# Performance work log

Measured on AMD Instinct MI355X. Metric: run time of the kernel, lower is better.

Reference implementation:

```python
import jax, jax.numpy as jnp
import numpy as np

N = 8192
E = 262144
IN_DIM = 128
OUT_DIM = 16


def _linear_params(key, fan_in, fan_out):
    k1, k2 = jax.random.split(key)
    bound = 1.0 / np.sqrt(fan_in)
    W = jax.random.uniform(k1, (fan_in, fan_out), jnp.float32, -bound, bound)
    b = jax.random.uniform(k2, (fan_out,), jnp.float32, -bound, bound)
    return W, b


def setup_inputs() -> dict:
    key = jax.random.key(0)
    ks = jax.random.split(key, 10)
    x = jax.random.normal(ks[0], (N, IN_DIM), jnp.float32)
    edge_index = jax.random.randint(ks[1], (2, E), 0, N, jnp.int64)
    W1, b1 = _linear_params(ks[2], IN_DIM, 128)
    W2, b2 = _linear_params(ks[3], 128, 256)
    W3, b3 = _linear_params(ks[4], 256, 64)
    Wk, bk = _linear_params(ks[5], 256, 256)
    Wq, bq = _linear_params(ks[6], 256, 256)
    Wr, br = _linear_params(ks[7], IN_DIM, 64)
    Wf, bf = _linear_params(ks[8], 64, OUT_DIM)
    ln_g = jnp.ones((64,), jnp.float32)
    ln_b = jnp.zeros((64,), jnp.float32)
    return dict(x=x, edge_index=edge_index, W1=W1, b1=b1, W2=W2, b2=b2,
                W3=W3, b3=b3, Wk=Wk, bk=bk, Wq=Wq, bq=bq, Wr=Wr, br=br,
                ln_g=ln_g, ln_b=ln_b, Wf=Wf, bf=bf)


def gcn_conv(x, W, b, row, col, n):
    # PyG GCNConv: add self-loops, symmetric normalization, aggregate src->dst
    xw = x @ W                                          # [N, F_out]
    loops = jnp.arange(n, dtype=row.dtype)
    r = jnp.concatenate([row, loops])
    c = jnp.concatenate([col, loops])
    deg = jax.ops.segment_sum(jnp.ones_like(c, jnp.float32), c, num_segments=n)
    dinv = jnp.where(deg > 0, jax.lax.rsqrt(jnp.maximum(deg, 1e-12)), 0.0)
    norm = dinv[r] * dinv[c]                            # [E+N]
    out = jax.ops.segment_sum(norm[:, None] * xw[r], c, num_segments=n)
    return out + b


def _forward(x, edge_index, W1, b1, W2, b2, W3, b3, Wk, bk, Wq, bq,
             Wr, br, ln_g, ln_b, Wf, bf):
    row, col = edge_index[0], edge_index[1]
    n = x.shape[0]
    residual = x @ Wr + br                              # [N, 64]
    h = jax.nn.leaky_relu(gcn_conv(x, W1, b1, row, col, n))   # dropout = eval no-op
    h = jax.nn.leaky_relu(gcn_conv(h, W2, b2, row, col, n))   # [N, 256]
    keys = h @ Wk + bk
    queries = h @ Wq + bq
    scores = queries @ keys.T                           # [N, N] dense, as in source
    mask = jnp.zeros((n, n), jnp.float32).at[row, col].set(1.0)
    scores = scores * mask                              # multiplicative mask (faithful)
    attn = jax.nn.softmax(scores, axis=-1)
    h = attn @ h                                        # [N, 256]
    h = jax.nn.leaky_relu(gcn_conv(h, W3, b3, row, col, n))   # [N, 64]
    z = h + residual
    mu = jnp.mean(z, axis=-1, keepdims=True)
    var = jnp.mean((z - mu) ** 2, axis=-1, keepdims=True)
    z = (z - mu) * jax.lax.rsqrt(var + 1e-5) * ln_g + ln_b
    pooled = jnp.max(z, axis=0)                         # 'max' pooling -> [64]
    return pooled @ Wf + bf                             # [OUT_DIM]


def reference(x, edge_index, W1, b1, W2, b2, W3, b3, Wk, bk, Wq, bq,
              Wr, br, ln_g, ln_b, Wf, bf):
    return _forward(x, edge_index, W1, b1, W2, b2, W3, b3, Wk, bk, Wq, bq,
                    Wr, br, ln_g, ln_b, Wf, bf)
```

## Files before the change

### kernel.cpp

```cpp
#include <hip/hip_runtime.h>
#include <hip/hip_fp16.h>
#include <cstdint>
#include <cstddef>

#define NNODES 8192
#define NEDGES 262144
#define MAXDEG 96
#define SMEM_BYTES 10496

typedef _Float16 f16x8 __attribute__((ext_vector_type(8)));
typedef _Float16 h2v   __attribute__((ext_vector_type(2)));
typedef float    f32x4 __attribute__((ext_vector_type(4)));

__device__ __forceinline__ float leaky(float v){ return v > 0.f ? v : 0.01f*v; }

__device__ __forceinline__ unsigned fmap(float f){
  unsigned u = __float_as_uint(f);
  return (u & 0x80000000u) ? ~u : (u | 0x80000000u);
}
__device__ __forceinline__ float funmap(unsigned u){
  return (u & 0x80000000u) ? __uint_as_float(u & 0x7FFFFFFFu) : __uint_as_float(~u);
}
__device__ __forceinline__ h2v as_h2(unsigned u){
  union{ unsigned x; h2v h; } c; c.x = u; return c.h;
}

struct GP {
  const float *x; const int *ei;
  const float *W1,*b1,*W2,*b2,*W3,*b3,*Wk,*bk,*Wq,*bq,*Wr,*br,*lng,*lnb,*Wf,*bfv;
  float* out;
  __half *xw1h,*h1h,*h1ah,*h2h,*qth,*gh,*hw3h;
  float *resid,*sw3;
  __half *Wqkt,*W2t,*W3t;
  float *bqk,*wb,*s0p;
  int *degc,*degr,*csrc,*csrd;
  unsigned* poolpart;
};

__device__ __forceinline__ void gemm_tile(const __half* __restrict__ A,
    const __half* __restrict__ Bt, const float* __restrict__ bias,
    float* __restrict__ Cf, __half* __restrict__ Ch, float* __restrict__ csum,
    int K, int N, int act, int bx, int by,
    _Float16 (*As)[40], _Float16 (*Bs)[40], float* cs){
  int t = threadIdx.x, w = t>>6, lane = t&63;
  int m0 = bx*64, n0 = by*64;
  int quad = lane>>4, l15 = lane&15;
  int srow = t>>2, soff = (t&3)*8;
  f32x4 acc0 = {0.f,0.f,0.f,0.f}, acc1 = acc0, acc2 = acc0, acc3 = acc0;
  for (int k0 = 0; k0 < K; k0 += 32){
    *(uint4*)&As[srow][soff] = *(const uint4*)(A  + (size_t)(m0+srow)*K + k0 + soff);
    *(uint4*)&Bs[srow][soff] = *(const uint4*)(Bt + (size_t)(n0+srow)*K + k0 + soff);
    __syncthreads();
    f16x8 af = *(const f16x8*)&As[w*16 + l15][quad*8];
    f16x8 b0 = *(const f16x8*)&Bs[ 0 + l15][quad*8];
    f16x8 b1 = *(const f16x8*)&Bs[16 + l15][quad*8];
    f16x8 b2 = *(const f16x8*)&Bs[32 + l15][quad*8];
    f16x8 b3 = *(const f16x8*)&Bs[48 + l15][quad*8];
    acc0 = __builtin_amdgcn_mfma_f32_16x16x32_f16(af, b0, acc0, 0,0,0);
    acc1 = __builtin_amdgcn_mfma_f32_16x16x32_f16(af, b1, acc1, 0,0,0);
    acc2 = __builtin_amdgcn_mfma_f32_16x16x32_f16(af, b2, acc2, 0,0,0);
    acc3 = __builtin_amdgcn_mfma_f32_16x16x32_f16(af, b3, acc3, 0,0,0);
    __syncthreads();
  }
  f32x4 accs[4] = {acc0, acc1, acc2, acc3};
  if (csum){
    if (t < 64) cs[t] = 0.f;
    __syncthreads();
    #pragma unroll
    for (int nt=0; nt<4; ++nt){
      float pp = accs[nt][0]+accs[nt][1]+accs[nt][2]+accs[nt][3];
      atomicAdd(&cs[nt*16 + l15], pp);
    }
    __syncthreads();
    if (t < 64) atomicAdd(&csum[n0 + t], cs[t]);
  }
  #pragma unroll
  for (int nt=0; nt<4; ++nt){
    int col = n0 + nt*16 + l15;
    float bv = bias ? bias[col] : 0.f;
    #pragma unroll
    for (int r=0;r<4;r++){
      int row = m0 + w*16 + quad*4 + r;
      float v = accs[nt][r] + bv;
      if (act) v = leaky(v);
      if (Cf) Cf[(size_t)row*N + col] = v;
      if (Ch) Ch[(size_t)row*N + col] = __float2half(v);
    }
  }
}

template<int TRANSB>
__device__ __forceinline__ void gemm_f32(const float* __restrict__ A,
    const float* __restrict__ B, const float* __restrict__ bias,
    float* __restrict__ Cf, __half* __restrict__ Ch,
    int K, int N, int bx, int by,
    _Float16 (*As)[40], _Float16 (*Bs)[40]){
  int t = threadIdx.x, w = t>>6, lane = t&63;
  int m0 = bx*64, n0 = by*64;
  int quad = lane>>4, l15 = lane&15;
  int srow = t>>2, soff = (t&3)*8;
  f32x4 acc0 = {0.f,0.f,0.f,0.f}, acc1 = acc0, acc2 = acc0, acc3 = acc0;
  for (int k0 = 0; k0 < K; k0 += 32){
    float4 a0 = *(const float4*)(A + (size_t)(m0+srow)*K + k0 + soff);
    float4 a1 = *(const float4*)(A + (size_t)(m0+srow)*K + k0 + soff + 4);
    _Float16* ad = &As[srow][soff];
    ad[0]=(_Float16)a0.x; ad[1]=(_Float16)a0.y; ad[2]=(_Float16)a0.z; ad[3]=(_Float16)a0.w;
    ad[4]=(_Float16)a1.x; ad[5]=(_Float16)a1.y; ad[6]=(_Float16)a1.z; ad[7]=(_Float16)a1.w;
    _Float16* bd = &Bs[srow][soff];
    if (TRANSB){
      #pragma unroll
      for (int u=0;u<8;u++)
        bd[u] = (_Float16)B[(size_t)(k0+soff+u)*N + n0+srow];
    } else {
      float4 b0 = *(const float4*)(B + (size_t)(n0+srow)*K + k0 + soff);
      float4 b1 = *(const float4*)(B + (size_t)(n0+srow)*K + k0 + soff + 4);
      bd[0]=(_Float16)b0.x; bd[1]=(_Float16)b0.y; bd[2]=(_Float16)b0.z; bd[3]=(_Float16)b0.w;
      bd[4]=(_Float16)b1.x; bd[5]=(_Float16)b1.y; bd[6]=(_Float16)b1.z; bd[7]=(_Float16)b1.w;
    }
    __syncthreads();
    f16x8 af = *(const f16x8*)&As[w*16 + l15][quad*8];
    f16x8 b0 = *(const f16x8*)&Bs[ 0 + l15][quad*8];
    f16x8 b1 = *(const f16x8*)&Bs[16 + l15][quad*8];
    f16x8 b2 = *(const f16x8*)&Bs[32 + l15][quad*8];
    f16x8 b3 = *(const f16x8*)&Bs[48 + l15][quad*8];
    acc0 = __builtin_amdgcn_mfma_f32_16x16x32_f16(af, b0, acc0, 0,0,0);
    acc1 = __builtin_amdgcn_mfma_f32_16x16x32_f16(af, b1, acc1, 0,0,0);
    acc2 = __builtin_amdgcn_mfma_f32_16x16x32_f16(af, b2, acc2, 0,0,0);
    acc3 = __builtin_amdgcn_mfma_f32_16x16x32_f16(af, b3, acc3, 0,0,0);
    __syncthreads();
  }
  f32x4 accs[4] = {acc0, acc1, acc2, acc3};
  #pragma unroll
  for (int nt=0; nt<4; ++nt){
    int col = n0 + nt*16 + l15;
    float bv = bias ? bias[col] : 0.f;
    #pragma unroll
    for (int r=0;r<4;r++){
      int row = m0 + w*16 + quad*4 + r;
      float v = accs[nt][r] + bv;
      if (Cf) Cf[(size_t)row*N + col] = v;
      if (Ch) Ch[(size_t)row*N + col] = __float2half(v);
    }
  }
}

template<int INS, int OUTS, int ACT>
__device__ __forceinline__ void agg128w(const __half* __restrict__ in,
    const int* __restrict__ deg, const int* __restrict__ src,
    __half* __restrict__ outp, const float* __restrict__ bias, int i){
  int lane = threadIdx.x & 63;
  int dcc = deg[i];
  float dc = rsqrtf((float)(dcc+1));
  int e0 = i*MAXDEG, e1 = e0 + dcc;
  float2 acc = make_float2(0.f, 0.f);
  for (int eb = e0; eb < e1; eb += 8){
    int m = e1 - eb; if (m > 8) m = 8;
    int r[8];
    #pragma unroll
    for (int u=0;u<8;u++) r[u] = src[(u<m) ? eb+u : eb];
    __half2 hv[8]; float sc[8];
    #pragma unroll
    for (int u=0;u<8;u++){
      hv[u] = *(const __half2*)(in + (size_t)r[u]*128 + lane*2);
      sc[u] = INS ? 1.f : rsqrtf((float)(deg[r[u]]+1));
    }
    #pragma unroll
    for (int u=0;u<8;u++){
      if (u < m){
        float2 h = __half22float2(hv[u]);
        if (INS){ acc.x += h.x; acc.y += h.y; }
        else { acc.x = fmaf(sc[u], h.x, acc.x); acc.y = fmaf(sc[u], h.y, acc.y); }
      }
    }
  }
  float2 self = __half22float2(*(const __half2*)(in + (size_t)i*128 + lane*2));
  float ss = INS ? 1.f : dc;
  float ox = dc*(ss*self.x + acc.x);
  float oy = dc*(ss*self.y + acc.y);
  if (ACT){
    ox = leaky(ox + bias[lane*2]);
    oy = leaky(oy + bias[lane*2+1]);
  }
  if (OUTS){ ox *= dc; oy *= dc; }
  *(__half2*)(outp + (size_t)i*128 + lane*2) = __floats2half2_rn(ox, oy);
}

__device__ __forceinline__ void attn_unit(const GP& p, int u){
  const int n = NNODES;
  int w = threadIdx.x>>6, lane = threadIdx.x&63;
  int i = u*4 + w;
  int fo = lane*4;
  uint2 qtu = *(const uint2*)(p.qth + (size_t)i*256 + fo);
  h2v q0 = as_h2(qtu.x), q1 = as_h2(qtu.y);
  float4 wbv = *(const float4*)(p.wb + fo);
  uint2 hiu  = *(const uint2*)(p.h2h + (size_t)i*256 + fo);
  float2 hia = __half22float2(*(__half2*)&hiu.x);
  float2 hib = __half22float2(*(__half2*)&hiu.y);
  float pv = hia.x*wbv.x + hia.y*wbv.y + hib.x*wbv.z + hib.y*wbv.w;
  #pragma unroll
  for (int mm=32; mm; mm>>=1) pv += __shfl_xor(pv, mm, 64);
  float base = pv + p.s0p[0];
  int dri = p.degr[i];
  int e0 = i*MAXDEG, e1 = e0 + dri;
  float acc = 0.f, dsum = 0.f;
  int slot = lane & 7;
  for (int eb = e0; eb < e1; eb += 8){
    int m = e1 - eb; if (m > 8) m = 8;
    int j[8];
    #pragma unroll
    for (int u8=0;u8<8;u8++) j[u8] = p.csrd[(u8<m) ? eb+u8 : eb];
    uint2 hv[8]; float gv[8];
    #pragma unroll
    for (int u8=0;u8<8;u8++){
      hv[u8] = *(const uint2*)(p.h2h + (size_t)j[u8]*256 + fo);
      gv[u8] = __half2float(p.gh[(size_t)j[u8]*64 + lane]);
    }
    float d[8];
    #pragma unroll
    for (int u8=0;u8<8;u8++)
      d[u8] = __builtin_amdgcn_fdot2(q1, as_h2(hv[u8].y),
              __builtin_amdgcn_fdot2(q0, as_h2(hv[u8].x), 0.f, false), false);
    #pragma unroll
    for (int v=0;v<8;v++) d[v] += __shfl_xor(d[v], 1, 64);
    float e0_ = (lane&1) ? d[1] : d[0];
    float e1_ = (lane&1) ? d[3] : d[2];
    float e2_ = (lane&1) ? d[5] : d[4];
    float e3_ = (lane&1) ? d[7] : d[6];
    e0_ += __shfl_xor(e0_, 2, 64);  e1_ += __shfl_xor(e1_, 2, 64);
    e2_ += __shfl_xor(e2_, 2, 64);  e3_ += __shfl_xor(e3_, 2, 64);
    float f0_ = (lane&2) ? e1_ : e0_;
    float f1_ = (lane&2) ? e3_ : e2_;
    f0_ += __shfl_xor(f0_, 4, 64);  f1_ += __shfl_xor(f1_, 4, 64);
    float g_ = (lane&4) ? f1_ : f0_;
    g_ += __shfl_xor(g_,  8, 64);
    g_ += __shfl_xor(g_, 16, 64);
    g_ += __shfl_xor(g_, 32, 64);
    float wep = __expf(g_ + base);
    float wm = (slot < m) ? wep : 0.f;
    wm += __shfl_xor(wm, 1, 64);
    wm += __shfl_xor(wm, 2, 64);
    wm += __shfl_xor(wm, 4, 64);
    dsum += wm;
    #pragma unroll
    for (int u8=0;u8<8;u8++){
      if (u8 < m){
        float wu = __shfl(wep, u8, 64);
        acc = fmaf(wu - 1.f, gv[u8], acc);
      }
    }
  }
  float inv = 1.0f / ((float)(n - dri) + dsum);
  float di = rsqrtf((float)(p.degc[i]+1));
  p.hw3h[(size_t)i*64 + lane] = __float2half(di * (p.sw3[lane] + acc) * inv);
}

__device__ __forceinline__ unsigned zp_val(const GP& p, int c){
  int lane = threadIdx.x & 63;
  int dcc = p.degc[c];
  float dc = rsqrtf((float)(dcc+1));
  float acc = 0.f;
  int e0 = c*MAXDEG, e1 = e0 + dcc;
  for (int eb = e0; eb < e1; eb += 8){
    int m = e1 - eb; if (m > 8) m = 8;
    int r[8];
    #pragma unroll
    for (int u=0;u<8;u++) r[u] = p.csrc[(u<m) ? eb+u : eb];
    __half hval[8];
    #pragma unroll
    for (int u=0;u<8;u++) hval[u] = p.hw3h[(size_t)r[u]*64 + lane];
    #pragma unroll
    for (int u=0;u<8;u++)
      if (u < m) acc += __half2float(hval[u]);
  }
  float self = __half2float(p.hw3h[(size_t)c*64 + lane]);
  float v = leaky(dc*(self + acc) + p.b3[lane]) + p.resid[(size_t)c*64 + lane];
  float s = v;
  #pragma unroll
  for (int mm=32; mm; mm>>=1) s += __shfl_xor(s, mm, 64);
  float mu = s * (1.0f/64.0f);
  float d = v - mu;
  float s2 = d*d;
  #pragma unroll
  for (int mm=32; mm; mm>>=1) s2 += __shfl_xor(s2, mm, 64);
  float zv = d * rsqrtf(s2*(1.0f/64.0f) + 1e-5f) * p.lng[lane] + p.lnb[lane];
  return fmap(zv);
}

__device__ __forceinline__ void final_unit(const GP& p, char* smem){
  int t = threadIdx.x, f = t & 63, g = t >> 6;
  unsigned (*sm)[64] = (unsigned(*)[64])smem;
  float* pool = (float*)(smem + 1024);
  unsigned mu = 0u;
  for (int b = g; b < 64; b += 4) mu = max(mu, p.poolpart[b*64 + f]);
  sm[g][f] = mu;
  __syncthreads();
  if (g == 0)
    pool[f] = funmap(max(max(sm[0][f],sm[1][f]), max(sm[2][f],sm[3][f])));
  __syncthreads();
  if (t < 16){
    float a = p.bfv[t];
    #pragma unroll
    for (int ff=0; ff<64; ++ff) a = fmaf(pool[ff], p.Wf[ff*16 + t], a);
    p.out[t] = a;
  }
}

__global__ __launch_bounds__(256) void k_z(GP p){
  __shared__ float smv[768];
  int b = blockIdx.x, t = threadIdx.x;
  if (b < 16){
    int idx = b*256 + t;
    int4 z = {0,0,0,0};
    ((int4*)p.degc)[idx] = z;
  } else if (b < 144){
    int idx = (b-16)*256 + t;
    int nn = idx >> 7, k = idx & 127;
    p.W2t[idx] = __float2half(p.W2[k*256 + nn]);
  } else if (b < 208){
    int idx = (b-144)*256 + t;
    int nn = idx >> 8, k = idx & 255;
    p.W3t[idx] = __float2half(p.W3[k*64 + nn]);
  } else if (b < 224){
    p.poolpart[(b-208)*256 + t] = 0u;
  } else if (b == 224){
    if (t < 64) p.sw3[t] = 0.f;
  } else {
    int c = b - 225;
    float* ra = smv; float* rb = smv + 256; float* rc = smv + 512;
    ra[t] = p.Wk[c*256 + t] * p.bq[t];
    rb[t] = p.Wq[c*256 + t] * p.bk[t];
    if (c == 0) rc[t] = p.bq[t]*p.bk[t];
    __syncthreads();
    for (int off=128; off; off>>=1){
      if (t < off){
        ra[t] += ra[t+off];
        rb[t] += rb[t+off];
        if (c == 0) rc[t] += rc[t+off];
      }
      __syncthreads();
    }
    if (t == 0){
      p.bqk[c] = ra[0];
      p.wb[c]  = rb[0];
      if (c == 0) p.s0p[0] = rc[0];
    }
  }
}

__global__ __launch_bounds__(256) void k_pre(GP p){
  __shared__ __align__(16) char smem[SMEM_BYTES];
  _Float16 (*As)[40] = (_Float16(*)[40])smem;
  _Float16 (*Bs)[40] = (_Float16(*)[40])(smem + 5120);
  int b = blockIdx.x, t = threadIdx.x;
  if (b < 1024){
    int e = b*256 + t;
    int r = p.ei[e], c = p.ei[NEDGES+e];
    int p1 = atomicAdd(&p.degc[c],1); p.csrc[c*MAXDEG + p1] = r;
    int p2 = atomicAdd(&p.degr[r],1); p.csrd[r*MAXDEG + p2] = c;
  } else if (b < 1280){
    int bb = b - 1024;
    gemm_f32<1>(p.x, p.W1, nullptr, nullptr, p.xw1h, 128, 128, bb>>1, bb&1, As, Bs);
  } else if (b < 1296){
    int bb = b - 1280;
    gemm_f32<0>(p.Wk, p.Wq, nullptr, nullptr, p.Wqkt, 256, 256, bb&3, bb>>2, As, Bs);
  } else {
    gemm_f32<1>(p.x, p.Wr, p.br, p.resid, nullptr, 128, 64, b-1296, 0, As, Bs);
  }
}

__global__ __launch_bounds__(256) void k_agg0(GP p){
  int i = blockIdx.x*4 + (threadIdx.x>>6);
  agg128w<0,1,1>(p.xw1h, p.degc, p.csrc, p.h1h, p.b1, i);
}
__global__ __launch_bounds__(256) void k_agg1(GP p){
  int i = blockIdx.x*4 + (threadIdx.x>>6);
  agg128w<1,0,0>(p.h1h, p.degc, p.csrc, p.h1ah, nullptr, i);
}

__global__ __launch_bounds__(256) void k_gemm2(GP p){
  __shared__ __align__(16) char smem[SMEM_BYTES];
  _Float16 (*As)[40] = (_Float16(*)[40])smem;
  _Float16 (*Bs)[40] = (_Float16(*)[40])(smem + 5120);
  int b = blockIdx.x;
  gemm_tile(p.h1ah, p.W2t, p.b2, nullptr, p.h2h, nullptr, 128, 256, 1, b>>2, b&3, As, Bs, nullptr);
}

__global__ __launch_bounds__(256) void k_mix2(GP p){
  __shared__ __align__(16) char smem[SMEM_BYTES];
  _Float16 (*As)[40] = (_Float16(*)[40])smem;
  _Float16 (*Bs)[40] = (_Float16(*)[40])(smem + 5120);
  float* cs = (float*)(smem + 10240);
  int b = blockIdx.x;
  if (b < 128) gemm_tile(p.h2h, p.W3t, nullptr, nullptr, p.gh, p.sw3, 256, 64, 0, b, 0, As, Bs, cs);
  else {
    int bb = b - 128;
    gemm_tile(p.h2h, p.Wqkt, p.bqk, nullptr, p.qth, nullptr, 256, 256, 0, bb>>2, bb&3, As, Bs, cs);
  }
}

__global__ __launch_bounds__(256) void k_attn(GP p){ attn_unit(p, blockIdx.x); }

__global__ __launch_bounds__(256) void k_zp(GP p){
  __shared__ unsigned red[4][64];
  int w = threadIdx.x>>6, lane = threadIdx.x&63;
  int c = blockIdx.x*4 + w;
  red[w][lane] = zp_val(p, c);
  __syncthreads();
  if (w == 0){
    unsigned m0 = max(max(red[0][lane], red[1][lane]),
                      max(red[2][lane], red[3][lane]));
    atomicMax(&p.poolpart[(blockIdx.x & 63)*64 + lane], m0);
  }
}

__global__ __launch_bounds__(256) void k_final(GP p){
  __shared__ __align__(16) char smem[SMEM_BYTES];
  final_unit(p, smem);
}

extern "C" void kernel_launch(void* const* d_in, const int* in_sizes, int n_in,
                              void* d_out, int out_size, void* d_ws, size_t ws_size,
                              hipStream_t stream){
  const int n = NNODES, E = NEDGES;
  char* ws = (char*)d_ws; size_t off = 0;
  auto alloc = [&](size_t bytes)->void*{
    void* pp = ws + off; off += (bytes + 255) & ~(size_t)255; return pp;
  };
  GP p;
  p.x   = (const float*)d_in[0];
  p.ei  = (const int*)d_in[1];
  p.W1  = (const float*)d_in[2];  p.b1 = (const float*)d_in[3];
  p.W2  = (const float*)d_in[4];  p.b2 = (const float*)d_in[5];
  p.W3  = (const float*)d_in[6];  p.b3 = (const float*)d_in[7];
  p.Wk  = (const float*)d_in[8];  p.bk = (const float*)d_in[9];
  p.Wq  = (const float*)d_in[10]; p.bq = (const float*)d_in[11];
  p.Wr  = (const float*)d_in[12]; p.br = (const float*)d_in[13];
  p.lng = (const float*)d_in[14]; p.lnb = (const float*)d_in[15];
  p.Wf  = (const float*)d_in[16]; p.bfv = (const float*)d_in[17];
  p.out = (float*)d_out;

  p.degc = (int*)alloc((size_t)n*4);
  p.degr = (int*)alloc((size_t)n*4);
  p.xw1h = (__half*)alloc((size_t)n*128*2);
  p.h1h  = (__half*)alloc((size_t)n*128*2);
  p.h1ah = (__half*)alloc((size_t)n*128*2);
  p.h2h  = (__half*)alloc((size_t)n*256*2);
  p.qth  = (__half*)alloc((size_t)n*256*2);
  p.gh   = (__half*)alloc((size_t)n*64*2);
  p.hw3h = (__half*)alloc((size_t)n*64*2);
  p.resid= (float*)alloc((size_t)n*64*4);
  p.sw3  = (float*)alloc(64*4);
  p.Wqkt = (__half*)alloc(256*256*2);
  p.W2t  = (__half*)alloc(128*256*2);
  p.W3t  = (__half*)alloc(256*64*2);
  p.bqk  = (float*)alloc(256*4);
  p.wb   = (float*)alloc(256*4);
  p.s0p  = (float*)alloc(4);
  p.csrc = (int*)alloc((size_t)n*MAXDEG*4);
  p.csrd = (int*)alloc((size_t)n*MAXDEG*4);
  p.poolpart = (unsigned*)alloc(64*64*4);

  k_z    <<<dim3(481),  256, 0, stream>>>(p);
  k_pre  <<<dim3(1424), 256, 0, stream>>>(p);
  k_agg0 <<<dim3(n/4),  256, 0, stream>>>(p);
  k_agg1 <<<dim3(n/4),  256, 0, stream>>>(p);
  k_gemm2<<<dim3(512),  256, 0, stream>>>(p);
  k_mix2 <<<dim3(640),  256, 0, stream>>>(p);
  k_attn <<<dim3(n/4),  256, 0, stream>>>(p);
  k_zp   <<<dim3(n/4),  256, 0, stream>>>(p);
  k_final<<<dim3(1),    256, 0, stream>>>(p);
}
```

Measured before the change: 204.8 us.

## Fuse final pooling into zp kernel via last-block counter; tile weight transposes

```diff
diff --git a/kernel.cpp b/kernel.cpp
--- a/kernel.cpp
+++ b/kernel.cpp
@@ -34,7 +34,7 @@
   __half *Wqkt,*W2t,*W3t;
   float *bqk,*wb,*s0p;
   int *degc,*degr,*csrc,*csrd;
-  unsigned* poolpart;
+  unsigned* poolpart; unsigned* donecnt;
 };
 
 __device__ __forceinline__ void gemm_tile(const __half* __restrict__ A,
@@ -286,12 +286,11 @@
   return fmap(zv);
 }
 
-__device__ __forceinline__ void final_unit(const GP& p, char* smem){
+__device__ __forceinline__ void final_unit(const GP& p, unsigned (*sm)[64], float* pool){
   int t = threadIdx.x, f = t & 63, g = t >> 6;
-  unsigned (*sm)[64] = (unsigned(*)[64])smem;
-  float* pool = (float*)(smem + 1024);
   unsigned mu = 0u;
-  for (int b = g; b < 64; b += 4) mu = max(mu, p.poolpart[b*64 + f]);
+  for (int b = g; b < 64; b += 4)
+    mu = max(mu, atomicOr(&p.poolpart[b*64 + f], 0u));
   sm[g][f] = mu;
   __syncthreads();
   if (g == 0)
@@ -307,25 +306,47 @@
 
 __global__ __launch_bounds__(256) void k_z(GP p){
   __shared__ float smv[768];
+  __shared__ _Float16 ts[64][66];
   int b = blockIdx.x, t = threadIdx.x;
+  int r4 = t>>6, cl = t&63;
   if (b < 16){
     int idx = b*256 + t;
     int4 z = {0,0,0,0};
     ((int4*)p.degc)[idx] = z;
-  } else if (b < 144){
-    int idx = (b-16)*256 + t;
-    int nn = idx >> 7, k = idx & 127;
-    p.W2t[idx] = __float2half(p.W2[k*256 + nn]);
-  } else if (b < 208){
-    int idx = (b-144)*256 + t;
-    int nn = idx >> 8, k = idx & 255;
-    p.W3t[idx] = __float2half(p.W3[k*64 + nn]);
-  } else if (b < 224){
-    p.poolpart[(b-208)*256 + t] = 0u;
-  } else if (b == 224){
+  } else if (b < 24){
+    int tt = b - 16;
+    int k0 = (tt>>2)*64, n0 = (tt&3)*64;
+    #pragma unroll
+    for (int q=0;q<16;q++){
+      int row = q*4 + r4;
+      ts[row][cl] = (_Float16)p.W2[(size_t)(k0+row)*256 + n0+cl];
+    }
+    __syncthreads();
+    #pragma unroll
+    for (int q=0;q<16;q++){
+      int row = q*4 + r4;
+      p.W2t[(size_t)(n0+row)*128 + k0+cl] = *(__half*)&ts[cl][row];
+    }
+  } else if (b < 28){
+    int k0 = (b-24)*64;
+    #pragma unroll
+    for (int q=0;q<16;q++){
+      int row = q*4 + r4;
+      ts[row][cl] = (_Float16)p.W3[(size_t)(k0+row)*64 + cl];
+    }
+    __syncthreads();
+    #pragma unroll
+    for (int q=0;q<16;q++){
+      int row = q*4 + r4;
+      p.W3t[(size_t)row*256 + k0+cl] = *(__half*)&ts[cl][row];
+    }
+  } else if (b < 44){
+    p.poolpart[(b-28)*256 + t] = 0u;
+  } else if (b == 44){
     if (t < 64) p.sw3[t] = 0.f;
+    else if (t == 64) *p.donecnt = 0u;
   } else {
-    int c = b - 225;
+    int c = b - 45;
     float* ra = smv; float* rb = smv + 256; float* rc = smv + 512;
     ra[t] = p.Wk[c*256 + t] * p.bq[t];
     rb[t] = p.Wq[c*256 + t] * p.bk[t];
@@ -387,9 +408,9 @@
 
 __global__ __launch_bounds__(256) void k_mix2(GP p){
   __shared__ __align__(16) char smem[SMEM_BYTES];
+  __shared__ float cs[64];
   _Float16 (*As)[40] = (_Float16(*)[40])smem;
   _Float16 (*Bs)[40] = (_Float16(*)[40])(smem + 5120);
-  float* cs = (float*)(smem + 10240);
   int b = blockIdx.x;
   if (b < 128) gemm_tile(p.h2h, p.W3t, nullptr, nullptr, p.gh, p.sw3, 256, 64, 0, b, 0, As, Bs, cs);
   else {
@@ -400,8 +421,10 @@
 
 __global__ __launch_bounds__(256) void k_attn(GP p){ attn_unit(p, blockIdx.x); }
 
-__global__ __launch_bounds__(256) void k_zp(GP p){
+__global__ __launch_bounds__(256) void k_zpf(GP p){
   __shared__ unsigned red[4][64];
+  __shared__ float pool[64];
+  __shared__ int lastflag;
   int w = threadIdx.x>>6, lane = threadIdx.x&63;
   int c = blockIdx.x*4 + w;
   red[w][lane] = zp_val(p, c);
@@ -410,12 +433,14 @@
     unsigned m0 = max(max(red[0][lane], red[1][lane]),
                       max(red[2][lane], red[3][lane]));
     atomicMax(&p.poolpart[(blockIdx.x & 63)*64 + lane], m0);
-  }
-}
-
-__global__ __launch_bounds__(256) void k_final(GP p){
-  __shared__ __align__(16) char smem[SMEM_BYTES];
-  final_unit(p, smem);
+    asm volatile("s_waitcnt vmcnt(0)" ::: "memory");
+    if (lane == 0){
+      unsigned oldc = atomicAdd(p.donecnt, 1u);
+      lastflag = (oldc == (unsigned)(NNODES/4 - 1));
+    }
+  }
+  __syncthreads();
+  if (lastflag) final_unit(p, red, pool);
 }
 
 extern "C" void kernel_launch(void* const* d_in, const int* in_sizes, int n_in,
@@ -459,14 +484,14 @@
   p.csrc = (int*)alloc((size_t)n*MAXDEG*4);
   p.csrd = (int*)alloc((size_t)n*MAXDEG*4);
   p.poolpart = (unsigned*)alloc(64*64*4);
-
-  k_z    <<<dim3(481),  256, 0, stream>>>(p);
+  p.donecnt  = (unsigned*)alloc(4);
+
+  k_z    <<<dim3(301),  256, 0, stream>>>(p);
   k_pre  <<<dim3(1424), 256, 0, stream>>>(p);
   k_agg0 <<<dim3(n/4),  256, 0, stream>>>(p);
   k_agg1 <<<dim3(n/4),  256, 0, stream>>>(p);
   k_gemm2<<<dim3(512),  256, 0, stream>>>(p);
   k_mix2 <<<dim3(640),  256, 0, stream>>>(p);
   k_attn <<<dim3(n/4),  256, 0, stream>>>(p);
-  k_zp   <<<dim3(n/4),  256, 0, stream>>>(p);
-  k_final<<<dim3(1),    256, 0, stream>>>(p);
-}
+  k_zpf  <<<dim3(n/4),  256, 0, stream>>>(p);
+}
```

Result: slower. 223.4 us (+9.1%).
